# Optimization experiments

Measured on AMD Instinct MI355X. Metric: run time of the kernel, lower is better.

## Reference

```python
import jax, jax.numpy as jnp
import numpy as np

EPS = 1e-5

def layernorm(x, w, b):
    mu = jnp.mean(x, axis=-1, keepdims=True)
    xc = x - mu
    var = jnp.mean(xc * xc, axis=-1, keepdims=True)
    return xc * jax.lax.rsqrt(var + EPS) * w + b

def setup_inputs() -> dict:
    key = jax.random.key(0)
    ks = jax.random.split(key, 9)
    B, T, Nm, Nl = 8, 8, 1024, 64
    Vw, Tw, H, Dh = 1024, 2048, 8, 64
    inner = H * Dh  # 512
    s_q = 1.0 / np.sqrt(Tw)
    s_kv = 1.0 / np.sqrt(Vw)
    s_o = 1.0 / np.sqrt(inner)
    return {
        "x": jax.random.normal(ks[0], (B, T, Nm, Vw), jnp.float32),
        "latents": jax.random.normal(ks[1], (B, T, Nl, Tw), jnp.float32),
        "nm_w": jnp.ones((Vw,), jnp.float32),
        "nm_b": jnp.zeros((Vw,), jnp.float32),
        "nl_w": jnp.ones((Tw,), jnp.float32),
        "nl_b": jnp.zeros((Tw,), jnp.float32),
        "Wq": jax.random.normal(ks[2], (Tw, inner), jnp.float32) * s_q,
        "Wkv": jax.random.normal(ks[3], (Vw, 2 * inner), jnp.float32) * s_kv,
        "Wout": jax.random.normal(ks[4], (inner, Tw), jnp.float32) * s_o,
    }

def reference(x, latents, nm_w, nm_b, nl_w, nl_b, Wq, Wkv, Wout):
    H, Dh = 8, 64
    scale = Dh ** (-0.5)
    B, T, Nm, _ = x.shape
    Nl = latents.shape[2]
    xn = layernorm(x, nm_w, nm_b)          # (B,T,Nm,Vw)
    ln = layernorm(latents, nl_w, nl_b)    # (B,T,Nl,Tw)
    q = (ln @ Wq).reshape(B, T, Nl, H, Dh)           # b t i h d
    kv = xn @ Wkv                                     # (B,T,Nm,2*inner)
    k, v = jnp.split(kv, 2, axis=-1)
    k = k.reshape(B, T, Nm, H, Dh)                    # b t j h d
    v = v.reshape(B, T, Nm, H, Dh)
    sim = jnp.einsum('btihd,btjhd->bthij', q * scale, k)  # (B,T,H,Nl,Nm)
    attn = jax.nn.softmax(sim, axis=-1)
    out = jnp.einsum('bthij,btjhd->btihd', attn, v)       # (B,T,Nl,H,Dh)
    out = out.reshape(B, T, Nl, H * Dh)
    return out @ Wout                                     # (B,T,Nl,Tw)
```

## Files before the change

kernel.cpp:

```cpp
#include <hip/hip_runtime.h>

typedef __attribute__((ext_vector_type(8))) short bfrag8;
typedef __attribute__((ext_vector_type(4))) float f32x4;

typedef const unsigned int __attribute__((address_space(1)))* gas1_u32;
typedef unsigned int __attribute__((address_space(3)))* gas3_u32;

#define DEV __device__ __forceinline__

DEV unsigned short f2bf(float f) {
  unsigned int u = __builtin_bit_cast(unsigned int, f);
  u += 0x7fffu + ((u >> 16) & 1u);
  return (unsigned short)(u >> 16);
}

DEV void gload_lds16(const void* g, void* l) {
  __builtin_amdgcn_global_load_lds((gas1_u32)g, (gas3_u32)l, 16, 0, 0);
}

template<int N> DEV void gate_bar();
template<> DEV void gate_bar<4>() { asm volatile("s_waitcnt vmcnt(4)\n\ts_barrier" ::: "memory"); }
template<> DEV void gate_bar<6>() { asm volatile("s_waitcnt vmcnt(6)\n\ts_barrier" ::: "memory"); }
template<> DEV void gate_bar<8>() { asm volatile("s_waitcnt vmcnt(8)\n\ts_barrier" ::: "memory"); }

__global__ __launch_bounds__(256) void k_xstats(
    const float* __restrict__ x, unsigned short* __restrict__ xb,
    float* __restrict__ mu, float* __restrict__ rstd)
{
  const int wid = threadIdx.x >> 6, lane = threadIdx.x & 63;
  const int row = blockIdx.x * 4 + wid;
  const float* base = x + (size_t)row * 1024;
  float4 v[4];
  #pragma unroll
  for (int i = 0; i < 4; ++i) v[i] = ((const float4*)base)[i * 64 + lane];
  float s = 0.f, q = 0.f;
  #pragma unroll
  for (int i = 0; i < 4; ++i) {
    s += v[i].x + v[i].y + v[i].z + v[i].w;
    q += v[i].x*v[i].x + v[i].y*v[i].y + v[i].z*v[i].z + v[i].w*v[i].w;
  }
  #pragma unroll
  for (int off = 32; off >= 1; off >>= 1) { s += __shfl_xor(s, off); q += __shfl_xor(q, off); }
  const float m  = s * (1.0f/1024.0f);
  const float var = q * (1.0f/1024.0f) - m * m;
  const float rs = rsqrtf(var + 1e-5f);
  if (lane == 0) { mu[row] = m; rstd[row] = rs; }
  unsigned short* ob = xb + (size_t)row * 1024;
  #pragma unroll
  for (int i = 0; i < 4; ++i) {
    ushort4 o;
    o.x = f2bf(v[i].x); o.y = f2bf(v[i].y); o.z = f2bf(v[i].z); o.w = f2bf(v[i].w);
    ((ushort4*)ob)[i * 64 + lane] = o;
  }
}

__global__ __launch_bounds__(256) void k_lnlat(
    const float* __restrict__ lat, const float* __restrict__ w,
    const float* __restrict__ b, unsigned short* __restrict__ ln)
{
  const int row = blockIdx.x, tid = threadIdx.x;
  const float* base = lat + (size_t)row * 2048;
  const float4 v0 = ((const float4*)base)[tid];
  const float4 v1 = ((const float4*)base)[256 + tid];
  float s = v0.x+v0.y+v0.z+v0.w + v1.x+v1.y+v1.z+v1.w;
  float q = v0.x*v0.x+v0.y*v0.y+v0.z*v0.z+v0.w*v0.w
          + v1.x*v1.x+v1.y*v1.y+v1.z*v1.z+v1.w*v1.w;
  #pragma unroll
  for (int off = 32; off >= 1; off >>= 1) { s += __shfl_xor(s, off); q += __shfl_xor(q, off); }
  __shared__ float red[8];
  const int wid = tid >> 6, lane = tid & 63;
  if (lane == 0) { red[wid] = s; red[4 + wid] = q; }
  __syncthreads();
  s = red[0] + red[1] + red[2] + red[3];
  q = red[4] + red[5] + red[6] + red[7];
  const float m  = s * (1.0f/2048.0f);
  const float var = q * (1.0f/2048.0f) - m * m;
  const float rs = rsqrtf(var + 1e-5f);
  const float4 w0 = ((const float4*)w)[tid], w1 = ((const float4*)w)[256 + tid];
  const float4 b0 = ((const float4*)b)[tid], b1 = ((const float4*)b)[256 + tid];
  ushort4 o0, o1;
  o0.x = f2bf((v0.x - m) * rs * w0.x + b0.x);
  o0.y = f2bf((v0.y - m) * rs * w0.y + b0.y);
  o0.z = f2bf((v0.z - m) * rs * w0.z + b0.z);
  o0.w = f2bf((v0.w - m) * rs * w0.w + b0.w);
  o1.x = f2bf((v1.x - m) * rs * w1.x + b1.x);
  o1.y = f2bf((v1.y - m) * rs * w1.y + b1.y);
  o1.z = f2bf((v1.z - m) * rs * w1.z + b1.z);
  o1.w = f2bf((v1.w - m) * rs * w1.w + b1.w);
  ((ushort4*)(ln + (size_t)row * 2048))[tid] = o0;
  ((ushort4*)(ln + (size_t)row * 2048))[256 + tid] = o1;
}

__global__ __launch_bounds__(256) void k_transpose_cast(
    const float* __restrict__ src, unsigned short* __restrict__ dst,
    int K, int N, const float* __restrict__ rowscale, float scale)
{
  __shared__ float tile[32][33];
  const int tx = threadIdx.x & 31, ty = threadIdx.x >> 5;
  const int ntiles = N >> 5;
  const int k0 = (blockIdx.x / ntiles) << 5;
  const int n0 = (blockIdx.x % ntiles) << 5;
  #pragma unroll
  for (int r = 0; r < 4; ++r) {
    const int kk = ty + r * 8;
    float v = src[(size_t)(k0 + kk) * N + n0 + tx] * scale;
    if (rowscale) v *= rowscale[k0 + kk];
    tile[kk][tx] = v;
  }
  __syncthreads();
  #pragma unroll
  for (int r = 0; r < 4; ++r) {
    const int nn = ty + r * 8;
    dst[(size_t)(n0 + nn) * K + k0 + tx] = f2bf(tile[tx][nn]);
  }
}

__global__ __launch_bounds__(256) void k_c1c2_part(
    const float* __restrict__ Wkv, const float* __restrict__ w,
    const float* __restrict__ b, float* __restrict__ part)
{
  const int kc = blockIdx.x;
  const int n  = blockIdx.y * 256 + threadIdx.x;
  float s1 = 0.f, s2 = 0.f;
  const int k0 = kc * 64;
  for (int k = k0; k < k0 + 64; ++k) {
    const float wv = Wkv[(size_t)k * 1024 + n];
    s1 += w[k] * wv;
    s2 += b[k] * wv;
  }
  part[(size_t)(kc * 2 + 0) * 1024 + n] = s1;
  part[(size_t)(kc * 2 + 1) * 1024 + n] = s2;
}

__global__ __launch_bounds__(256) void k_c1c2_red(
    const float* __restrict__ part, float* __restrict__ c1, float* __restrict__ c2)
{
  const int n = blockIdx.x * 256 + threadIdx.x;
  float s1 = 0.f, s2 = 0.f;
  #pragma unroll
  for (int kc = 0; kc < 16; ++kc) {
    s1 += part[(size_t)(kc * 2 + 0) * 1024 + n];
    s2 += part[(size_t)(kc * 2 + 1) * 1024 + n];
  }
  c1[n] = s1; c2[n] = s2;
}

#define BAR8   __builtin_amdgcn_s_barrier()
#define GATE4  gate_bar<4>()

__global__ __launch_bounds__(512, 2) void k_gemm8(
    const unsigned short* __restrict__ A,
    const unsigned short* __restrict__ Bt,
    unsigned short* __restrict__ C,
    const float* __restrict__ mu, const float* __restrict__ rstd,
    const float* __restrict__ c1, const float* __restrict__ c2)
{
  constexpr int NKT = 16;
  __shared__ __attribute__((aligned(16))) char lds[131072];

  int bid = blockIdx.x;
  { const int nwg = gridDim.x; const int q = nwg >> 3; bid = (bid & 7) * q + (bid >> 3); }
  const int mt = bid >> 2, nt = bid & 3;
  const int tid = threadIdx.x;
  const int wid = tid >> 6, lane = tid & 63;
  const int g = lane >> 4, c = lane & 15;
  const int wr = wid >> 2, wc = wid & 3;
  const int MO = wr * 128, NO = wc * 64;

  const unsigned short* gA = A + (size_t)mt * 256 * 1024;
  const unsigned short* gB = Bt + (size_t)nt * 256 * 1024;

  const f32x4 zz = {0.f, 0.f, 0.f, 0.f};
  f32x4 acc[8][4];
  #pragma unroll
  for (int m = 0; m < 8; ++m)
    #pragma unroll
    for (int n = 0; n < 4; ++n) acc[m][n] = zz;

  auto stageA = [&](int buf, int kk, int kt) {
    #pragma unroll
    for (int i = 0; i < 2; ++i) {
      const int o = (i * 512 + tid) * 16;
      const int row = o >> 6;
      const int ss = ((((o >> 4) & 3) - (row >> 1)) & 3);
      gload_lds16((const char*)(gA + (size_t)row * 1024 + kt * 64 + kk * 32) + ss * 16,
                  lds + buf * 32768 + kk * 16384 + o);
    }
  };
  auto stageB = [&](int buf, int kk, int kt) {
    #pragma unroll
    for (int i = 0; i < 2; ++i) {
      const int o = (i * 512 + tid) * 16;
      const int row = o >> 6;
      const int ss = ((((o >> 4) & 3) - (row >> 1)) & 3);
      gload_lds16((const char*)(gB + (size_t)row * 1024 + kt * 64 + kk * 32) + ss * 16,
                  lds + 65536 + buf * 32768 + kk * 16384 + o);
    }
  };
  auto rdA = [&](int buf, int kk, int m) -> bfrag8 {
    const int row = MO + m * 16 + c;
    return *(const bfrag8*)(lds + buf * 32768 + kk * 16384 + row * 64
                            + (((g + (row >> 1)) & 3) << 4));
  };
  auto rdB = [&](int buf, int kk, int n) -> bfrag8 {
    const int row = NO + n * 16 + c;
    return *(const bfrag8*)(lds + 65536 + buf * 32768 + kk * 16384 + row * 64
                            + (((g + (row >> 1)) & 3) << 4));
  };

  bfrag8 a[8], b0[4], b1[4];

  auto tile4 = [&](int buf, int sb, int ukt) {
    #pragma unroll
    for (int m = 0; m < 8; ++m) a[m] = rdA(buf, 0, m);
    #pragma unroll
    for (int n = 0; n < 4; ++n) b0[n] = rdB(buf, 0, n);
    stageA(sb, 0, ukt);
    __builtin_amdgcn_s_setprio(1);
    #pragma unroll
    for (int m = 0; m < 8; ++m) {
      acc[m][0] = __builtin_amdgcn_mfma_f32_16x16x32_bf16(a[m], b0[0], acc[m][0], 0, 0, 0);
      acc[m][1] = __builtin_amdgcn_mfma_f32_16x16x32_bf16(a[m], b0[1], acc[m][1], 0, 0, 0);
    }
    __builtin_amdgcn_s_setprio(0);
    GATE4;
    #pragma unroll
    for (int n = 0; n < 4; ++n) b1[n] = rdB(buf, 1, n);
    stageB(sb, 0, ukt);
    __builtin_amdgcn_s_setprio(1);
    #pragma unroll
    for (int m = 0; m < 8; ++m) {
      acc[m][2] = __builtin_amdgcn_mfma_f32_16x16x32_bf16(a[m], b0[2], acc[m][2], 0, 0, 0);
      acc[m][3] = __builtin_amdgcn_mfma_f32_16x16x32_bf16(a[m], b0[3], acc[m][3], 0, 0, 0);
    }
    __builtin_amdgcn_s_setprio(0);
    GATE4;
    #pragma unroll
    for (int m = 0; m < 8; ++m) a[m] = rdA(buf, 1, m);
    stageB(sb, 1, ukt);
    __builtin_amdgcn_s_setprio(1);
    #pragma unroll
    for (int m = 0; m < 8; ++m) {
      acc[m][0] = __builtin_amdgcn_mfma_f32_16x16x32_bf16(a[m], b1[0], acc[m][0], 0, 0, 0);
      acc[m][1] = __builtin_amdgcn_mfma_f32_16x16x32_bf16(a[m], b1[1], acc[m][1], 0, 0, 0);
    }
    __builtin_amdgcn_s_setprio(0);
    BAR8;
    stageA(sb, 1, ukt);
    __builtin_amdgcn_s_setprio(1);
    #pragma unroll
    for (int m = 0; m < 8; ++m) {
      acc[m][2] = __builtin_amdgcn_mfma_f32_16x16x32_bf16(a[m], b1[2], acc[m][2], 0, 0, 0);
      acc[m][3] = __builtin_amdgcn_mfma_f32_16x16x32_bf16(a[m], b1[3], acc[m][3], 0, 0, 0);
    }
    __builtin_amdgcn_s_setprio(0);
    GATE4;
  };

  stageA(0, 0, 0); stageB(0, 0, 0); stageB(0, 1, 0); stageA(0, 1, 0);
  GATE4;

  for (int t = 0; t < NKT; t += 2) {
    const int u2 = (t + 2 < NKT) ? t + 2 : 0;
    tile4(0, 1, t + 1);
    tile4(1, 0, u2);
  }
  asm volatile("s_waitcnt vmcnt(0)" ::: "memory");

  #pragma unroll
  for (int m = 0; m < 8; ++m) {
    #pragma unroll
    for (int j = 0; j < 4; ++j) {
      const size_t orow = (size_t)mt * 256 + MO + m * 16 + g * 4 + j;
      const float rs = rstd[orow], muv = mu[orow];
      #pragma unroll
      for (int n = 0; n < 4; ++n) {
        const int gcol = nt * 256 + NO + n * 16 + c;
        const float v = rs * (acc[m][n][j] - muv * c1[gcol]) + c2[gcol];
        C[orow * 1024 + gcol] = f2bf(v);
      }
    }
  }
}

template<int BM, int BN, int WM, int WN, int NT, int MODE>
__global__ __launch_bounds__(NT, 2) void k_gemm(
    const unsigned short* __restrict__ A, int lda,
    const unsigned short* __restrict__ Bt, int ldb,
    int K, int mtiles, int ntiles,
    void* __restrict__ Cout, int ldc)
{
  constexpr int BK = 32;
  constexpr int NW = NT / 64;
  constexpr int MF = (BM / WM) / 16;
  constexpr int NF = (BN / WN) / 16;
  constexpr int LA = (BM * BK) / (8 * NT);
  constexpr int LB = (BN * BK) / (8 * NT);
  constexpr int LPS = LA + LB;
  constexpr int RA = BM * BK;
  constexpr int RB = BN * BK;
  static_assert(WM * WN == NW, "wave grid");
  static_assert(LA >= 1 && LB >= 1, "tile too small for NT");
  static_assert(LPS == 3 || LPS == 4, "gate specialization");

  __shared__ __attribute__((aligned(16))) unsigned short As[4 * RA];
  __shared__ __attribute__((aligned(16))) unsigned short Bs[4 * RB];

  int bid = blockIdx.x;
  {
    const int nwg = gridDim.x;
    if ((nwg & 7) == 0) {
      const int q = nwg >> 3;
      bid = (bid & 7) * q + (bid >> 3);
    }
  }
  const int mt = bid / ntiles, nt = bid % ntiles;
  const int tid = threadIdx.x;
  const int wid = tid >> 6, lane = tid & 63;
  const int g = lane >> 4, c = lane & 15;
  const int wr = wid / WN, wc = wid % WN;
  const int MO = wr * (BM / WM), NO = wc * (BN / WN);
  const int rot = (c >> 1) & 3;

  const unsigned short* gA = A + (size_t)mt * BM * lda;
  const unsigned short* gB = Bt + (size_t)nt * BN * ldb;

  const f32x4 zz = {0.f, 0.f, 0.f, 0.f};
  f32x4 acc[MF][NF];
  #pragma unroll
  for (int m = 0; m < MF; ++m)
    #pragma unroll
    for (int n = 0; n < NF; ++n) acc[m][n] = zz;

  auto stage = [&](int R, int kt) {
    #pragma unroll
    for (int i = 0; i < LA; ++i) {
      const int o = (i * NT + tid) * 16;
      const int row = o >> 6;
      const int slot = (o >> 4) & 3;
      const int srcb = (((slot - ((row >> 1) & 3)) & 3) << 4);
      gload_lds16((const char*)(gA + (size_t)row * lda + kt * BK) + srcb,
                  (char*)(As + R * RA) + o);
    }
    #pragma unroll
    for (int i = 0; i < LB; ++i) {
      const int o = (i * NT + tid) * 16;
      const int row = o >> 6;
      const int slot = (o >> 4) & 3;
      const int srcb = (((slot - ((row >> 1) & 3)) & 3) << 4);
      gload_lds16((const char*)(gB + (size_t)row * ldb + kt * BK) + srcb,
                  (char*)(Bs + R * RB) + o);
    }
  };

  auto compute = [&](int R) {
    const char* as = (const char*)(As + R * RA);
    const char* bs = (const char*)(Bs + R * RB);
    bfrag8 af[MF], bf[NF];
    #pragma unroll
    for (int m = 0; m < MF; ++m) {
      const int rw = MO + m * 16 + c;
      af[m] = *(const bfrag8*)(as + rw * 64 + (((g + rot) & 3) << 4));
    }
    #pragma unroll
    for (int n = 0; n < NF; ++n) {
      const int rw = NO + n * 16 + c;
      bf[n] = *(const bfrag8*)(bs + rw * 64 + (((g + rot) & 3) << 4));
    }
    #pragma unroll
    for (int m = 0; m < MF; ++m)
      #pragma unroll
      for (int n = 0; n < NF; ++n)
        acc[m][n] = __builtin_amdgcn_mfma_f32_16x16x32_bf16(af[m], bf[n], acc[m][n], 0, 0, 0);
  };

  const int nkt = K / BK;
  stage(0, 0); stage(1, 1); stage(2, 2);
  for (int t = 0; t < nkt; t += 4) {
    #pragma unroll
    for (int r = 0; r < 4; ++r) {
      int t3 = t + r + 3; if (t3 >= nkt) t3 -= nkt;
      gate_bar<2 * LPS>();
      stage((r + 3) & 3, t3);
      compute(r);
    }
  }
  asm volatile("s_waitcnt vmcnt(0)" ::: "memory");

  #pragma unroll
  for (int m = 0; m < MF; ++m) {
    #pragma unroll
    for (int j = 0; j < 4; ++j) {
      const size_t orow = (size_t)mt * BM + MO + m * 16 + g * 4 + j;
      #pragma unroll
      for (int n = 0; n < NF; ++n) {
        const int gcol = nt * BN + NO + n * 16 + c;
        const float v = acc[m][n][j];
        if constexpr (MODE == 2) ((float*)Cout)[orow * ldc + gcol] = v;
        else ((unsigned short*)Cout)[orow * ldc + gcol] = f2bf(v);
      }
    }
  }
}

__global__ __launch_bounds__(256) void k_attn(
    const unsigned short* __restrict__ q,
    const unsigned short* __restrict__ kv,
    unsigned short* __restrict__ ao)
{
  __shared__ __attribute__((aligned(16))) unsigned short Vt[64 * 64];
  const int bid = blockIdx.x;
  const int bt = bid >> 3, h = bid & 7;
  const int tid = threadIdx.x;
  const int wid = tid >> 6, lane = tid & 63;
  const int g = lane >> 4, c = lane & 15;

  const size_t qoff = ((size_t)bt * 64 + wid * 16 + c) * 512 + h * 64;
  const bfrag8 qf0 = *(const bfrag8*)(q + qoff + g * 8);
  const bfrag8 qf1 = *(const bfrag8*)(q + qoff + 32 + g * 8);

  const f32x4 zz = {0.f, 0.f, 0.f, 0.f};
  f32x4 o[4] = {zz, zz, zz, zz};
  float m_run = -1e30f, l_run = 0.f;

  const size_t kvbase = (size_t)bt * 1024 * 1024;
  const unsigned short* kbase = kv + kvbase + h * 64;
  const unsigned short* vbase = kv + kvbase + 512 + h * 64;

  for (int ch = 0; ch < 16; ++ch) {
    #pragma unroll
    for (int rr = 0; rr < 2; ++rr) {
      const int key = rr * 32 + (tid >> 3);
      const int d0 = (tid & 7) * 8;
      const bfrag8 vv = *(const bfrag8*)(vbase + (size_t)(ch * 64 + key) * 1024 + d0);
      #pragma unroll
      for (int j = 0; j < 8; ++j)
        Vt[(d0 + j) * 64 + (key ^ (j << 3))] = (unsigned short)vv[j];
    }
    __syncthreads();
    #pragma unroll
    for (int ks = 0; ks < 2; ++ks) {
      const int kb = ch * 64 + ks * 32;
      f32x4 s[2];
      #pragma unroll
      for (int t = 0; t < 2; ++t) {
        const int kr = ((c >> 2) << 3) + (t << 2) + (c & 3);
        const unsigned short* krow = kbase + (size_t)(kb + kr) * 1024;
        s[t] = zz;
        s[t] = __builtin_amdgcn_mfma_f32_16x16x32_bf16(*(const bfrag8*)(krow + g * 8),      qf0, s[t], 0, 0, 0);
        s[t] = __builtin_amdgcn_mfma_f32_16x16x32_bf16(*(const bfrag8*)(krow + 32 + g * 8), qf1, s[t], 0, 0, 0);
      }
      float pm = s[0][0];
      #pragma unroll
      for (int i = 1; i < 4; ++i) pm = fmaxf(pm, s[0][i]);
      #pragma unroll
      for (int i = 0; i < 4; ++i) pm = fmaxf(pm, s[1][i]);
      pm = fmaxf(pm, __shfl_xor(pm, 16));
      pm = fmaxf(pm, __shfl_xor(pm, 32));
      const float mn = fmaxf(m_run, pm);
      const float alpha = __expf(m_run - mn);
      float p[8];
      #pragma unroll
      for (int i = 0; i < 4; ++i) p[i]     = __expf(s[0][i] - mn);
      #pragma unroll
      for (int i = 0; i < 4; ++i) p[4 + i] = __expf(s[1][i] - mn);
      float ts = 0.f;
      #pragma unroll
      for (int i = 0; i < 8; ++i) ts += p[i];
      ts += __shfl_xor(ts, 16);
      ts += __shfl_xor(ts, 32);
      l_run = l_run * alpha + ts;
      m_run = mn;
      float ar[4];
      #pragma unroll
      for (int rj = 0; rj < 4; ++rj) ar[rj] = __shfl(alpha, g * 4 + rj);
      #pragma unroll
      for (int db = 0; db < 4; ++db)
        #pragma unroll
        for (int j = 0; j < 4; ++j) o[db][j] *= ar[j];
      bfrag8 pa;
      #pragma unroll
      for (int i = 0; i < 8; ++i) pa[i] = (short)f2bf(p[i]);
      #pragma unroll
      for (int db = 0; db < 4; ++db) {
        const int d = db * 16 + c;
        const bfrag8 vb = *(const bfrag8*)(Vt + d * 64 + ((ks * 32 + g * 8) ^ ((c & 7) << 3)));
        o[db] = __builtin_amdgcn_mfma_f32_16x16x32_bf16(pa, vb, o[db], 0, 0, 0);
      }
    }
    __syncthreads();
  }
  float lr[4];
  #pragma unroll
  for (int rj = 0; rj < 4; ++rj) lr[rj] = __shfl(l_run, g * 4 + rj);
  #pragma unroll
  for (int db = 0; db < 4; ++db)
    #pragma unroll
    for (int j = 0; j < 4; ++j) {
      const float val = o[db][j] / lr[j];
      ao[((size_t)bt * 64 + wid * 16 + g * 4 + j) * 512 + h * 64 + db * 16 + c] = f2bf(val);
    }
}

extern "C" void kernel_launch(void* const* d_in, const int* in_sizes, int n_in,
                              void* d_out, int out_size, void* d_ws, size_t ws_size,
                              hipStream_t stream)
{
  const float* x    = (const float*)d_in[0];
  const float* lat  = (const float*)d_in[1];
  const float* nm_w = (const float*)d_in[2];
  const float* nm_b = (const float*)d_in[3];
  const float* nl_w = (const float*)d_in[4];
  const float* nl_b = (const float*)d_in[5];
  const float* Wq   = (const float*)d_in[6];
  const float* Wkv  = (const float*)d_in[7];
  const float* Wout = (const float*)d_in[8];

  char* p = (char*)d_ws;
  auto take = [&](size_t bytes) { char* r = p; p += (bytes + 255) & ~(size_t)255; return r; };
  unsigned short* xb    = (unsigned short*)take(64ull * 1024 * 1024 * 2);
  unsigned short* kvb   = (unsigned short*)take(64ull * 1024 * 1024 * 2);
  unsigned short* lnb   = (unsigned short*)take(4096ull * 2048 * 2);
  unsigned short* qbuf  = (unsigned short*)take(4096ull * 512 * 2);
  unsigned short* aob   = (unsigned short*)take(4096ull * 512 * 2);
  unsigned short* WqT   = (unsigned short*)take(512ull * 2048 * 2);
  unsigned short* WkvT  = (unsigned short*)take(1024ull * 1024 * 2);
  unsigned short* WoutT = (unsigned short*)take(2048ull * 512 * 2);
  float* muv  = (float*)take(65536ull * 4);
  float* rsd  = (float*)take(65536ull * 4);
  float* c1   = (float*)take(1024 * 4);
  float* c2   = (float*)take(1024 * 4);
  float* part = (float*)take(32ull * 1024 * 4);
  if ((size_t)(p - (char*)d_ws) > ws_size) return;

  k_transpose_cast<<<dim3(64 * 16), 256, 0, stream>>>(Wq,   WqT,   2048,  512, nullptr, 0.125f);
  k_transpose_cast<<<dim3(32 * 32), 256, 0, stream>>>(Wkv,  WkvT,  1024, 1024, nm_w,    1.0f);
  k_transpose_cast<<<dim3(16 * 64), 256, 0, stream>>>(Wout, WoutT,  512, 2048, nullptr, 1.0f);
  k_c1c2_part<<<dim3(16, 4), 256, 0, stream>>>(Wkv, nm_w, nm_b, part);
  k_c1c2_red<<<dim3(4), 256, 0, stream>>>(part, c1, c2);
  k_xstats<<<dim3(16384), 256, 0, stream>>>(x, xb, muv, rsd);
  k_lnlat<<<dim3(4096), 256, 0, stream>>>(lat, nl_w, nl_b, lnb);

  k_gemm8<<<dim3(1024), 512, 0, stream>>>(xb, WkvT, kvb, muv, rsd, c1, c2);
  k_gemm<64, 128, 1, 4, 256, 1><<<dim3(256), 256, 0, stream>>>(
      lnb, 2048, WqT, 2048, 2048, 64, 4, qbuf, 512);

  k_attn<<<dim3(512), 256, 0, stream>>>(qbuf, kvb, aob);

  k_gemm<64, 128, 1, 4, 256, 2><<<dim3(1024), 256, 0, stream>>>(
      aob, 512, WoutT, 512, 512, 64, 16, d_out, 2048);
}
```

Baseline: 378.3 us.

## Merge preprocessing kernels into one launch and rework generic GEMM to BK=64 double buffer

Folds the x-stats, latent layernorm, three weight transpose-casts and c1/c2 partial-sum kernels into a single k_pre launch that dispatches on block index, cutting launch overhead and tail gaps between small kernels. Separately, the generic k_gemm moves from a 4-stage BK=32 ring with vmcnt-gated barriers to a 2-buffer BK=64 pipeline with __syncthreads and a new XOR-style LDS swizzle. This reduces barrier count per K but loses deeper prefetch, so load latency may be less hidden in the Q and output projections.

```diff
diff --git a/kernel.cpp b/kernel.cpp
--- a/kernel.cpp
+++ b/kernel.cpp
@@ -18,118 +18,120 @@
   __builtin_amdgcn_global_load_lds((gas1_u32)g, (gas3_u32)l, 16, 0, 0);
 }
 
-template<int N> DEV void gate_bar();
-template<> DEV void gate_bar<4>() { asm volatile("s_waitcnt vmcnt(4)\n\ts_barrier" ::: "memory"); }
-template<> DEV void gate_bar<6>() { asm volatile("s_waitcnt vmcnt(6)\n\ts_barrier" ::: "memory"); }
-template<> DEV void gate_bar<8>() { asm volatile("s_waitcnt vmcnt(8)\n\ts_barrier" ::: "memory"); }
-
-__global__ __launch_bounds__(256) void k_xstats(
+__global__ __launch_bounds__(256) void k_pre(
     const float* __restrict__ x, unsigned short* __restrict__ xb,
-    float* __restrict__ mu, float* __restrict__ rstd)
+    float* __restrict__ mu, float* __restrict__ rstd,
+    const float* __restrict__ lat, const float* __restrict__ nl_w,
+    const float* __restrict__ nl_b, unsigned short* __restrict__ lnb,
+    const float* __restrict__ Wq,   unsigned short* __restrict__ WqT,
+    const float* __restrict__ Wkv,  unsigned short* __restrict__ WkvT,
+    const float* __restrict__ Wout, unsigned short* __restrict__ WoutT,
+    const float* __restrict__ nm_w, const float* __restrict__ nm_b,
+    float* __restrict__ part)
 {
-  const int wid = threadIdx.x >> 6, lane = threadIdx.x & 63;
-  const int row = blockIdx.x * 4 + wid;
-  const float* base = x + (size_t)row * 1024;
-  float4 v[4];
-  #pragma unroll
-  for (int i = 0; i < 4; ++i) v[i] = ((const float4*)base)[i * 64 + lane];
-  float s = 0.f, q = 0.f;
-  #pragma unroll
-  for (int i = 0; i < 4; ++i) {
-    s += v[i].x + v[i].y + v[i].z + v[i].w;
-    q += v[i].x*v[i].x + v[i].y*v[i].y + v[i].z*v[i].z + v[i].w*v[i].w;
-  }
-  #pragma unroll
-  for (int off = 32; off >= 1; off >>= 1) { s += __shfl_xor(s, off); q += __shfl_xor(q, off); }
-  const float m  = s * (1.0f/1024.0f);
-  const float var = q * (1.0f/1024.0f) - m * m;
-  const float rs = rsqrtf(var + 1e-5f);
-  if (lane == 0) { mu[row] = m; rstd[row] = rs; }
-  unsigned short* ob = xb + (size_t)row * 1024;
-  #pragma unroll
-  for (int i = 0; i < 4; ++i) {
-    ushort4 o;
-    o.x = f2bf(v[i].x); o.y = f2bf(v[i].y); o.z = f2bf(v[i].z); o.w = f2bf(v[i].w);
-    ((ushort4*)ob)[i * 64 + lane] = o;
-  }
-}
-
-__global__ __launch_bounds__(256) void k_lnlat(
-    const float* __restrict__ lat, const float* __restrict__ w,
-    const float* __restrict__ b, unsigned short* __restrict__ ln)
-{
-  const int row = blockIdx.x, tid = threadIdx.x;
-  const float* base = lat + (size_t)row * 2048;
-  const float4 v0 = ((const float4*)base)[tid];
-  const float4 v1 = ((const float4*)base)[256 + tid];
-  float s = v0.x+v0.y+v0.z+v0.w + v1.x+v1.y+v1.z+v1.w;
-  float q = v0.x*v0.x+v0.y*v0.y+v0.z*v0.z+v0.w*v0.w
-          + v1.x*v1.x+v1.y*v1.y+v1.z*v1.z+v1.w*v1.w;
-  #pragma unroll
-  for (int off = 32; off >= 1; off >>= 1) { s += __shfl_xor(s, off); q += __shfl_xor(q, off); }
-  __shared__ float red[8];
+  __shared__ float smem[32 * 33];
+  const int bid = blockIdx.x, tid = threadIdx.x;
   const int wid = tid >> 6, lane = tid & 63;
-  if (lane == 0) { red[wid] = s; red[4 + wid] = q; }
-  __syncthreads();
-  s = red[0] + red[1] + red[2] + red[3];
-  q = red[4] + red[5] + red[6] + red[7];
-  const float m  = s * (1.0f/2048.0f);
-  const float var = q * (1.0f/2048.0f) - m * m;
-  const float rs = rsqrtf(var + 1e-5f);
-  const float4 w0 = ((const float4*)w)[tid], w1 = ((const float4*)w)[256 + tid];
-  const float4 b0 = ((const float4*)b)[tid], b1 = ((const float4*)b)[256 + tid];
-  ushort4 o0, o1;
-  o0.x = f2bf((v0.x - m) * rs * w0.x + b0.x);
-  o0.y = f2bf((v0.y - m) * rs * w0.y + b0.y);
-  o0.z = f2bf((v0.z - m) * rs * w0.z + b0.z);
-  o0.w = f2bf((v0.w - m) * rs * w0.w + b0.w);
-  o1.x = f2bf((v1.x - m) * rs * w1.x + b1.x);
-  o1.y = f2bf((v1.y - m) * rs * w1.y + b1.y);
-  o1.z = f2bf((v1.z - m) * rs * w1.z + b1.z);
-  o1.w = f2bf((v1.w - m) * rs * w1.w + b1.w);
-  ((ushort4*)(ln + (size_t)row * 2048))[tid] = o0;
-  ((ushort4*)(ln + (size_t)row * 2048))[256 + tid] = o1;
-}
-
-__global__ __launch_bounds__(256) void k_transpose_cast(
-    const float* __restrict__ src, unsigned short* __restrict__ dst,
-    int K, int N, const float* __restrict__ rowscale, float scale)
-{
-  __shared__ float tile[32][33];
-  const int tx = threadIdx.x & 31, ty = threadIdx.x >> 5;
-  const int ntiles = N >> 5;
-  const int k0 = (blockIdx.x / ntiles) << 5;
-  const int n0 = (blockIdx.x % ntiles) << 5;
-  #pragma unroll
-  for (int r = 0; r < 4; ++r) {
-    const int kk = ty + r * 8;
-    float v = src[(size_t)(k0 + kk) * N + n0 + tx] * scale;
-    if (rowscale) v *= rowscale[k0 + kk];
-    tile[kk][tx] = v;
-  }
-  __syncthreads();
-  #pragma unroll
-  for (int r = 0; r < 4; ++r) {
-    const int nn = ty + r * 8;
-    dst[(size_t)(n0 + nn) * K + k0 + tx] = f2bf(tile[tx][nn]);
-  }
-}
-
-__global__ __launch_bounds__(256) void k_c1c2_part(
-    const float* __restrict__ Wkv, const float* __restrict__ w,
-    const float* __restrict__ b, float* __restrict__ part)
-{
-  const int kc = blockIdx.x;
-  const int n  = blockIdx.y * 256 + threadIdx.x;
-  float s1 = 0.f, s2 = 0.f;
-  const int k0 = kc * 64;
-  for (int k = k0; k < k0 + 64; ++k) {
-    const float wv = Wkv[(size_t)k * 1024 + n];
-    s1 += w[k] * wv;
-    s2 += b[k] * wv;
-  }
-  part[(size_t)(kc * 2 + 0) * 1024 + n] = s1;
-  part[(size_t)(kc * 2 + 1) * 1024 + n] = s2;
+
+  if (bid < 16384) {
+    const int row = bid * 4 + wid;
+    const float* base = x + (size_t)row * 1024;
+    float4 v[4];
+    #pragma unroll
+    for (int i = 0; i < 4; ++i) v[i] = ((const float4*)base)[i * 64 + lane];
+    float s = 0.f, q = 0.f;
+    #pragma unroll
+    for (int i = 0; i < 4; ++i) {
+      s += v[i].x + v[i].y + v[i].z + v[i].w;
+      q += v[i].x*v[i].x + v[i].y*v[i].y + v[i].z*v[i].z + v[i].w*v[i].w;
+    }
+    #pragma unroll
+    for (int off = 32; off >= 1; off >>= 1) { s += __shfl_xor(s, off); q += __shfl_xor(q, off); }
+    const float m  = s * (1.0f/1024.0f);
+    const float var = q * (1.0f/1024.0f) - m * m;
+    const float rs = rsqrtf(var + 1e-5f);
+    if (lane == 0) { mu[row] = m; rstd[row] = rs; }
+    unsigned short* ob = xb + (size_t)row * 1024;
+    #pragma unroll
+    for (int i = 0; i < 4; ++i) {
+      ushort4 o;
+      o.x = f2bf(v[i].x); o.y = f2bf(v[i].y); o.z = f2bf(v[i].z); o.w = f2bf(v[i].w);
+      ((ushort4*)ob)[i * 64 + lane] = o;
+    }
+    return;
+  }
+  if (bid < 20480) {
+    const int row = bid - 16384;
+    const float* base = lat + (size_t)row * 2048;
+    const float4 v0 = ((const float4*)base)[tid];
+    const float4 v1 = ((const float4*)base)[256 + tid];
+    float s = v0.x+v0.y+v0.z+v0.w + v1.x+v1.y+v1.z+v1.w;
+    float q = v0.x*v0.x+v0.y*v0.y+v0.z*v0.z+v0.w*v0.w
+            + v1.x*v1.x+v1.y*v1.y+v1.z*v1.z+v1.w*v1.w;
+    #pragma unroll
+    for (int off = 32; off >= 1; off >>= 1) { s += __shfl_xor(s, off); q += __shfl_xor(q, off); }
+    if (lane == 0) { smem[wid] = s; smem[4 + wid] = q; }
+    __syncthreads();
+    s = smem[0] + smem[1] + smem[2] + smem[3];
+    q = smem[4] + smem[5] + smem[6] + smem[7];
+    const float m  = s * (1.0f/2048.0f);
+    const float var = q * (1.0f/2048.0f) - m * m;
+    const float rs = rsqrtf(var + 1e-5f);
+    const float4 w0 = ((const float4*)nl_w)[tid], w1 = ((const float4*)nl_w)[256 + tid];
+    const float4 b0 = ((const float4*)nl_b)[tid], b1 = ((const float4*)nl_b)[256 + tid];
+    ushort4 o0, o1;
+    o0.x = f2bf((v0.x - m) * rs * w0.x + b0.x);
+    o0.y = f2bf((v0.y - m) * rs * w0.y + b0.y);
+    o0.z = f2bf((v0.z - m) * rs * w0.z + b0.z);
+    o0.w = f2bf((v0.w - m) * rs * w0.w + b0.w);
+    o1.x = f2bf((v1.x - m) * rs * w1.x + b1.x);
+    o1.y = f2bf((v1.y - m) * rs * w1.y + b1.y);
+    o1.z = f2bf((v1.z - m) * rs * w1.z + b1.z);
+    o1.w = f2bf((v1.w - m) * rs * w1.w + b1.w);
+    ((ushort4*)(lnb + (size_t)row * 2048))[tid] = o0;
+    ((ushort4*)(lnb + (size_t)row * 2048))[256 + tid] = o1;
+    return;
+  }
+  if (bid < 23552) {
+    int tb = bid - 20480;
+    const float* src; unsigned short* dst; int Kd, N; const float* rsc; float sc;
+    if (tb < 1024)      { src = Wq;   dst = WqT;   Kd = 2048; N = 512;  rsc = nullptr; sc = 0.125f; }
+    else if (tb < 2048) { tb -= 1024; src = Wkv;  dst = WkvT;  Kd = 1024; N = 1024; rsc = nm_w;   sc = 1.0f; }
+    else                { tb -= 2048; src = Wout; dst = WoutT; Kd = 512;  N = 2048; rsc = nullptr; sc = 1.0f; }
+    float (*tile)[33] = (float(*)[33])smem;
+    const int tx = tid & 31, ty = tid >> 5;
+    const int ntiles = N >> 5;
+    const int k0 = (tb / ntiles) << 5;
+    const int n0 = (tb % ntiles) << 5;
+    #pragma unroll
+    for (int r = 0; r < 4; ++r) {
+      const int kk = ty + r * 8;
+      float v = src[(size_t)(k0 + kk) * N + n0 + tx] * sc;
+      if (rsc) v *= rsc[k0 + kk];
+      tile[kk][tx] = v;
+    }
+    __syncthreads();
+    #pragma unroll
+    for (int r = 0; r < 4; ++r) {
+      const int nn = ty + r * 8;
+      dst[(size_t)(n0 + nn) * Kd + k0 + tx] = f2bf(tile[tx][nn]);
+    }
+    return;
+  }
+  {
+    const int cb = bid - 23552;
+    const int kc = cb >> 2;
+    const int n  = (cb & 3) * 256 + tid;
+    float s1 = 0.f, s2 = 0.f;
+    const int k0 = kc * 64;
+    for (int k = k0; k < k0 + 64; ++k) {
+      const float wv = Wkv[(size_t)k * 1024 + n];
+      s1 += nm_w[k] * wv;
+      s2 += nm_b[k] * wv;
+    }
+    part[(size_t)(kc * 2 + 0) * 1024 + n] = s1;
+    part[(size_t)(kc * 2 + 1) * 1024 + n] = s2;
+  }
 }
 
 __global__ __launch_bounds__(256) void k_c1c2_red(
@@ -146,7 +148,7 @@
 }
 
 #define BAR8   __builtin_amdgcn_s_barrier()
-#define GATE4  gate_bar<4>()
+#define GATE4  asm volatile("s_waitcnt vmcnt(4)\n\ts_barrier" ::: "memory")
 
 __global__ __launch_bounds__(512, 2) void k_gemm8(
     const unsigned short* __restrict__ A,
@@ -290,21 +292,17 @@
     int K, int mtiles, int ntiles,
     void* __restrict__ Cout, int ldc)
 {
-  constexpr int BK = 32;
+  constexpr int BK = 64;
   constexpr int NW = NT / 64;
   constexpr int MF = (BM / WM) / 16;
   constexpr int NF = (BN / WN) / 16;
   constexpr int LA = (BM * BK) / (8 * NT);
   constexpr int LB = (BN * BK) / (8 * NT);
-  constexpr int LPS = LA + LB;
-  constexpr int RA = BM * BK;
-  constexpr int RB = BN * BK;
   static_assert(WM * WN == NW, "wave grid");
   static_assert(LA >= 1 && LB >= 1, "tile too small for NT");
-  static_assert(LPS == 3 || LPS == 4, "gate specialization");
-
-  __shared__ __attribute__((aligned(16))) unsigned short As[4 * RA];
-  __shared__ __attribute__((aligned(16))) unsigned short Bs[4 * RB];
+
+  __shared__ __attribute__((aligned(16))) unsigned short As[2][BM * BK];
+  __shared__ __attribute__((aligned(16))) unsigned short Bs[2][BN * BK];
 
   int bid = blockIdx.x;
   {
@@ -320,7 +318,6 @@
   const int g = lane >> 4, c = lane & 15;
   const int wr = wid / WN, wc = wid % WN;
   const int MO = wr * (BM / WM), NO = wc * (BN / WN);
-  const int rot = (c >> 1) & 3;
 
   const unsigned short* gA = A + (size_t)mt * BM * lda;
   const unsigned short* gB = Bt + (size_t)nt * BN * ldb;
@@ -332,60 +329,60 @@
     #pragma unroll
     for (int n = 0; n < NF; ++n) acc[m][n] = zz;
 
-  auto stage = [&](int R, int kt) {
+  auto stage = [&](int buf, int kt) {
     #pragma unroll
     for (int i = 0; i < LA; ++i) {
       const int o = (i * NT + tid) * 16;
-      const int row = o >> 6;
-      const int slot = (o >> 4) & 3;
-      const int srcb = (((slot - ((row >> 1) & 3)) & 3) << 4);
-      gload_lds16((const char*)(gA + (size_t)row * lda + kt * BK) + srcb,
-                  (char*)(As + R * RA) + o);
+      const int row = o >> 7;
+      const int sg = (((o >> 4) & 7) - row) & 7;
+      gload_lds16((const char*)(gA + (size_t)row * lda + kt * BK) + sg * 16,
+                  (char*)&As[buf][0] + o);
     }
     #pragma unroll
     for (int i = 0; i < LB; ++i) {
       const int o = (i * NT + tid) * 16;
-      const int row = o >> 6;
-      const int slot = (o >> 4) & 3;
-      const int srcb = (((slot - ((row >> 1) & 3)) & 3) << 4);
-      gload_lds16((const char*)(gB + (size_t)row * ldb + kt * BK) + srcb,
-                  (char*)(Bs + R * RB) + o);
-    }
-  };
-
-  auto compute = [&](int R) {
-    const char* as = (const char*)(As + R * RA);
-    const char* bs = (const char*)(Bs + R * RB);
-    bfrag8 af[MF], bf[NF];
-    #pragma unroll
-    for (int m = 0; m < MF; ++m) {
-      const int rw = MO + m * 16 + c;
-      af[m] = *(const bfrag8*)(as + rw * 64 + (((g + rot) & 3) << 4));
-    }
-    #pragma unroll
-    for (int n = 0; n < NF; ++n) {
-      const int rw = NO + n * 16 + c;
-      bf[n] = *(const bfrag8*)(bs + rw * 64 + (((g + rot) & 3) << 4));
-    }
-    #pragma unroll
-    for (int m = 0; m < MF; ++m)
-      #pragma unroll
-      for (int n = 0; n < NF; ++n)
-        acc[m][n] = __builtin_amdgcn_mfma_f32_16x16x32_bf16(af[m], bf[n], acc[m][n], 0, 0, 0);
+      const int row = o >> 7;
+      const int sg = (((o >> 4) & 7) - row) & 7;
+      gload_lds16((const char*)(gB + (size_t)row * ldb + kt * BK) + sg * 16,
+                  (char*)&Bs[buf][0] + o);
+    }
+  };
+
+  auto compute = [&](int buf) {
+    #pragma unroll
+    for (int kk = 0; kk < 2; ++kk) {
+      bfrag8 af[MF], bf[NF];
+      #pragma unroll
+      for (int m = 0; m < MF; ++m) {
+        const int rw = MO + m * 16 + c;
+        af[m] = *(const bfrag8*)((const char*)&As[buf][0] + rw * 128
+                                 + (((kk * 4 + g + rw) & 7) << 4));
+      }
+      #pragma unroll
+      for (int n = 0; n < NF; ++n) {
+        const int rw = NO + n * 16 + c;
+        bf[n] = *(const bfrag8*)((const char*)&Bs[buf][0] + rw * 128
+                                 + (((kk * 4 + g + rw) & 7) << 4));
+      }
+      #pragma unroll
+      for (int m = 0; m < MF; ++m)
+        #pragma unroll
+        for (int n = 0; n < NF; ++n)
+          acc[m][n] = __builtin_amdgcn_mfma_f32_16x16x32_bf16(af[m], bf[n], acc[m][n], 0, 0, 0);
+    }
   };
 
   const int nkt = K / BK;
-  stage(0, 0); stage(1, 1); stage(2, 2);
-  for (int t = 0; t < nkt; t += 4) {
-    #pragma unroll
-    for (int r = 0; r < 4; ++r) {
-      int t3 = t + r + 3; if (t3 >= nkt) t3 -= nkt;
-      gate_bar<2 * LPS>();
-      stage((r + 3) & 3, t3);
-      compute(r);
-    }
-  }
-  asm volatile("s_waitcnt vmcnt(0)" ::: "memory");
+  stage(0, 0);
+  __syncthreads();
+  for (int t = 0; t < nkt; t += 2) {
+    if (t + 1 < nkt) stage(1, t + 1);
+    compute(0);
+    __syncthreads();
+    if (t + 2 < nkt) stage(0, t + 2);
+    if (t + 1 < nkt) compute(1);
+    __syncthreads();
+  }
 
   #pragma unroll
   for (int m = 0; m < MF; ++m) {
@@ -533,13 +530,11 @@
   float* part = (float*)take(32ull * 1024 * 4);
   if ((size_t)(p - (char*)d_ws) > ws_size) return;
 
-  k_transpose_cast<<<dim3(64 * 16), 256, 0, stream>>>(Wq,   WqT,   2048,  512, nullptr, 0.125f);
-  k_transpose_cast<<<dim3(32 * 32), 256, 0, stream>>>(Wkv,  WkvT,  1024, 1024, nm_w,    1.0f);
-  k_transpose_cast<<<dim3(16 * 64), 256, 0, stream>>>(Wout, WoutT,  512, 2048, nullptr, 1.0f);
-  k_c1c2_part<<<dim3(16, 4), 256, 0, stream>>>(Wkv, nm_w, nm_b, part);
+  k_pre<<<dim3(23616), 256, 0, stream>>>(x, xb, muv, rsd,
+                                         lat, nl_w, nl_b, lnb,
+                                         Wq, WqT, Wkv, WkvT, Wout, WoutT,
+                                         nm_w, nm_b, part);
   k_c1c2_red<<<dim3(4), 256, 0, stream>>>(part, c1, c2);
-  k_xstats<<<dim3(16384), 256, 0, stream>>>(x, xb, muv, rsd);
-  k_lnlat<<<dim3(4096), 256, 0, stream>>>(lat, nl_w, nl_b, lnb);
 
   k_gemm8<<<dim3(1024), 512, 0, stream>>>(xb, WkvT, kvb, muv, rsd, c1, c2);
   k_gemm<64, 128, 1, 4, 256, 1><<<dim3(256), 256, 0, stream>>>(
```

After: 363.0 us. 4.0% less time.
